# Kernel tuning notes

Measured on AMD Instinct MI355X. Metric: run time of the kernel, lower is better.

The kernel has to match this reference:

```python
import jax, jax.numpy as jnp
import numpy as np

B, S, D = 2, 2048, 1024
H = 8
HD = D // H  # 128
RANK = 4
CONTROL_SCALE = 1.0


def setup_inputs() -> dict:
    key = jax.random.key(0)
    ks = jax.random.split(key, 8)
    sd = 0.02
    return {
        "hidden_states": jax.random.normal(ks[0], (B, S, D), jnp.float32),
        "control_states": jax.random.normal(ks[1], (B, S, D), jnp.float32),
        "Wq": jax.random.normal(ks[2], (D, D), jnp.float32) * sd,
        "Wk": jax.random.normal(ks[3], (D, D), jnp.float32) * sd,
        "Wv": jax.random.normal(ks[4], (D, D), jnp.float32) * sd,
        "Wo": jax.random.normal(ks[5], (D, D), jnp.float32) * sd,
        "bo": jnp.zeros((D,), jnp.float32),
        "lora_down": jax.random.normal(ks[6], (RANK, D), jnp.float32) * sd,
        "lora_up": jax.random.normal(ks[7], (D, RANK), jnp.float32) * sd,
    }


def _split_heads(x):  # [B,S,D] -> [B,H,S,HD]
    return x.reshape(B, S, H, HD).transpose(0, 2, 1, 3)


def reference(hidden_states, control_states, Wq, Wk, Wv, Wo, bo, lora_down, lora_up):
    # q/k/v projections (Linear, no bias); self-attention (encoder_hidden_states=None)
    q = _split_heads(jnp.einsum("bsd,ed->bse", hidden_states, Wq))
    k = _split_heads(jnp.einsum("bsd,ed->bse", hidden_states, Wk))
    v = _split_heads(jnp.einsum("bsd,ed->bse", hidden_states, Wv))
    inv_sqrt_d = 1.0 / jnp.sqrt(jnp.asarray(HD, q.dtype))
    scores = jnp.einsum("bhqd,bhkd->bhqk", q, k) * inv_sqrt_d  # [B,H,S,S]
    probs = jax.nn.softmax(scores, axis=-1)
    attn_out = jnp.einsum("bhqk,bhkd->bhqd", probs, v)  # [B,H,S,HD]
    attn_out = attn_out.transpose(0, 2, 1, 3).reshape(B, S, D)
    # to_out[0] Linear with bias; to_out[1] Dropout is identity at eval
    out = jnp.einsum("bsd,ed->bse", attn_out, Wo) + bo
    # LoRA control injection: up(down(control_states))
    ctrl = jnp.einsum("bsr,er->bse", jnp.einsum("bsd,rd->bsr", control_states, lora_down), lora_up)
    return out + CONTROL_SCALE * ctrl
```

## Files before the change

### kernel.cpp

```cpp
#include <hip/hip_runtime.h>
#include <hip/hip_bf16.h>


typedef __bf16 bf8_t __attribute__((ext_vector_type(8)));
typedef float f32x4 __attribute__((ext_vector_type(4)));

#define MFMA_BF16(a, b, c) __builtin_amdgcn_mfma_f32_16x16x32_bf16((a), (b), (c), 0, 0, 0)

__device__ __forceinline__ void gload_lds16(const void* g, void* l) {
  __builtin_amdgcn_global_load_lds(
      (const __attribute__((address_space(1))) void*)g,
      (__attribute__((address_space(3))) void*)l, 16, 0, 0);
}

__global__ __launch_bounds__(256) void cvt5_k(
    const float* __restrict__ s0, const float* __restrict__ s1,
    const float* __restrict__ s2, const float* __restrict__ s3,
    const float* __restrict__ s4, __bf16* __restrict__ d0,
    __bf16* __restrict__ d1, __bf16* __restrict__ d2, __bf16* __restrict__ d3,
    __bf16* __restrict__ d4) {
  const int which = blockIdx.y;
  const float* s = (which == 0) ? s0 : (which == 1) ? s1 : (which == 2) ? s2
                   : (which == 3) ? s3 : s4;
  __bf16* d = (which == 0) ? d0 : (which == 1) ? d1 : (which == 2) ? d2
              : (which == 3) ? d3 : d4;
  const int n = (which == 0) ? (4096 * 1024) : (1024 * 1024);
  const int i = (blockIdx.x * 256 + threadIdx.x) * 8;
  if (i >= n) return;
  float4 a = *(const float4*)(s + i);
  float4 b = *(const float4*)(s + i + 4);
  bf8_t r;
  r[0] = (__bf16)a.x; r[1] = (__bf16)a.y; r[2] = (__bf16)a.z; r[3] = (__bf16)a.w;
  r[4] = (__bf16)b.x; r[5] = (__bf16)b.y; r[6] = (__bf16)b.z; r[7] = (__bf16)b.w;
  *(bf8_t*)(d + i) = r;
}

__device__ __forceinline__ void gemm_tile(const __bf16* __restrict__ Abase,
                                          const __bf16* __restrict__ Wbase,
                                          int K, __bf16* sA, __bf16* sB,
                                          f32x4 acc[4][4]) {
  const int tid = threadIdx.x;
  const int wave = tid >> 6, lane = tid & 63;
  const int wr = (wave >> 1) * 64, wc = (wave & 1) * 64;
  const int lrow = lane >> 3, lchunk = lane & 7;

  for (int m = 0; m < 4; ++m)
    for (int n = 0; n < 4; ++n)
      acc[m][n] = f32x4{0.f, 0.f, 0.f, 0.f};

  for (int k0 = 0; k0 < K; k0 += 64) {
    for (int i = 0; i < 4; ++i) {
      const int rbase = i * 32 + wave * 8;
      gload_lds16(Abase + (size_t)(rbase + lrow) * K + k0 + lchunk * 8,
                  sA + rbase * 64);
      gload_lds16(Wbase + (size_t)(rbase + lrow) * K + k0 + lchunk * 8,
                  sB + rbase * 64);
    }
    __syncthreads();

    for (int kk = 0; kk < 2; ++kk) {
      bf8_t af[4], bfr[4];
      const int koff = kk * 32 + (lane >> 4) * 8;
      for (int m = 0; m < 4; ++m)
        af[m] = *(const bf8_t*)&sA[(wr + m * 16 + (lane & 15)) * 64 + koff];
      for (int n = 0; n < 4; ++n)
        bfr[n] = *(const bf8_t*)&sB[(wc + n * 16 + (lane & 15)) * 64 + koff];
      for (int m = 0; m < 4; ++m)
        for (int n = 0; n < 4; ++n)
          acc[m][n] = MFMA_BF16(af[m], bfr[n], acc[m][n]);
    }
    __syncthreads();
  }
}

__global__ __launch_bounds__(256) void gemm_qkv_k(
    const __bf16* __restrict__ X, const __bf16* __restrict__ Wq,
    const __bf16* __restrict__ Wk, const __bf16* __restrict__ Wv,
    __bf16* __restrict__ Qb, __bf16* __restrict__ Kb, __bf16* __restrict__ Vtb) {
  __shared__ __bf16 sA[128 * 64];
  __shared__ __bf16 sB[128 * 64];
  const int z = blockIdx.z;
  const int K = 1024;
  int rowT, colT, Nout;
  const __bf16 *Abase, *Wbase;
  __bf16* C;
  if (z == 2) {
    rowT = blockIdx.x; colT = blockIdx.y; Nout = 4096;
    Abase = Wv + (size_t)rowT * 128 * K;
    Wbase = X + (size_t)colT * 128 * K;
    C = Vtb;
  } else {
    rowT = blockIdx.y; colT = blockIdx.x; Nout = 1024;
    Abase = X + (size_t)rowT * 128 * K;
    Wbase = ((z == 0) ? Wq : Wk) + (size_t)colT * 128 * K;
    C = (z == 0) ? Qb : Kb;
  }
  f32x4 acc[4][4];
  gemm_tile(Abase, Wbase, K, sA, sB, acc);

  const int lane = threadIdx.x & 63, wave = threadIdx.x >> 6;
  const int wr = (wave >> 1) * 64, wc = (wave & 1) * 64;
  const int row0 = rowT * 128 + wr + (lane >> 4) * 4;
  const int col0 = colT * 128 + wc + (lane & 15);
  for (int m = 0; m < 4; ++m)
    for (int n = 0; n < 4; ++n)
      for (int j = 0; j < 4; ++j)
        C[(size_t)(row0 + m * 16 + j) * Nout + col0 + n * 16] = (__bf16)acc[m][n][j];
}

__global__ __launch_bounds__(256) void lora_down_k(
    const float* __restrict__ ctrl, const float* __restrict__ down,
    float* __restrict__ tmp) {
  const int tid = threadIdx.x, wave = tid >> 6, lane = tid & 63;
  const int s = blockIdx.x * 4 + wave;
  const float* cp = ctrl + (size_t)s * 1024 + lane * 16;
  float4 c[4];
  for (int i = 0; i < 4; ++i) c[i] = *(const float4*)(cp + i * 4);
  for (int r = 0; r < 4; ++r) {
    const float* dp = down + r * 1024 + lane * 16;
    float acc = 0.f;
    for (int i = 0; i < 4; ++i) {
      float4 dv = *(const float4*)(dp + i * 4);
      acc += c[i].x * dv.x + c[i].y * dv.y + c[i].z * dv.z + c[i].w * dv.w;
    }
    for (int off = 32; off > 0; off >>= 1) acc += __shfl_xor(acc, off);
    if (lane == 0) tmp[s * 4 + r] = acc;
  }
}

__global__ __launch_bounds__(256) void flash_attn_k(
    const __bf16* __restrict__ Qg, const __bf16* __restrict__ Kg,
    const __bf16* __restrict__ Vtg, __bf16* __restrict__ Og) {
  const int S = 2048, D = 1024;
  __shared__ __bf16 sK[2][64 * 128];
  __shared__ __bf16 sVt[2][128 * 64];
  __shared__ __bf16 sP[4][16 * 72];
  const int qt = blockIdx.x, bh = blockIdx.y;
  const int b = bh >> 3, h = bh & 7;
  const int tid = threadIdx.x, wave = tid >> 6, lane = tid & 63;
  const size_t base = (size_t)b * S * D + (size_t)h * 128;
  const size_t vtbase = (size_t)h * 128 * 4096 + (size_t)b * 2048;
  const int q0 = qt * 64 + wave * 16;
  const int g = lane >> 4;
  const int koff = g * 8;

  bf8_t qf[4];
  {
    const float scale = 0.08838834764831845f;
    const __bf16* qp = Qg + base + (size_t)(q0 + (lane & 15)) * D + koff;
    for (int d0 = 0; d0 < 4; ++d0) {
      bf8_t v = *(const bf8_t*)(qp + d0 * 32);
      for (int j = 0; j < 8; ++j) v[j] = (__bf16)((float)v[j] * scale);
      qf[d0] = v;
    }
  }

  f32x4 o[8];
  for (int f = 0; f < 8; ++f) o[f] = f32x4{0.f, 0.f, 0.f, 0.f};
  float mrow[4] = {-1e30f, -1e30f, -1e30f, -1e30f};
  float lrow[4] = {0.f, 0.f, 0.f, 0.f};

  auto stageK = [&](int buf, int kv) {
    for (int i = 0; i < 4; ++i) {
      const int r = i * 16 + wave * 4 + (lane >> 4);
      const int gc = (lane & 15) ^ (r & 7);
      gload_lds16(Kg + base + (size_t)(kv + r) * D + gc * 8,
                  &sK[buf][i * 2048 + wave * 512]);
    }
  };
  auto stageV = [&](int buf, int kv) {
    for (int i = 0; i < 4; ++i) {
      const int r = wave * 32 + i * 8 + (lane >> 3);
      const int gc = (lane & 7) ^ (r & 7);
      gload_lds16(Vtg + vtbase + (size_t)r * 4096 + kv + gc * 8,
                  &sVt[buf][(wave * 32 + i * 8) * 64]);
    }
  };

  stageK(0, 0);
  stageV(0, 0);

  for (int t = 0; t < 32; ++t) {
    const int cur = t & 1;
    __syncthreads();
    if (t < 31) {
      stageK(cur ^ 1, (t + 1) * 64);
      stageV(cur ^ 1, (t + 1) * 64);
    }

    f32x4 s4[4];
    const __bf16* kb_ = sK[cur];
    for (int n = 0; n < 4; ++n) {
      f32x4 a_ = f32x4{0.f, 0.f, 0.f, 0.f};
      const int r = n * 16 + (lane & 15);
      for (int d0 = 0; d0 < 4; ++d0) {
        const int c = (4 * d0 + g) ^ (r & 7);
        a_ = MFMA_BF16(qf[d0], *(const bf8_t*)&kb_[r * 128 + c * 8], a_);
      }
      s4[n] = a_;
    }

    float tmax[4];
    for (int j = 0; j < 4; ++j)
      tmax[j] = fmaxf(fmaxf(s4[0][j], s4[1][j]), fmaxf(s4[2][j], s4[3][j]));
    for (int off = 1; off < 16; off <<= 1)
      for (int j = 0; j < 4; ++j)
        tmax[j] = fmaxf(tmax[j], __shfl_xor(tmax[j], off));
    float sc_[4], rs[4];
    for (int j = 0; j < 4; ++j) {
      float mnew = fmaxf(mrow[j], tmax[j]);
      sc_[j] = __expf(mrow[j] - mnew);
      mrow[j] = mnew;
      rs[j] = 0.f;
    }
    for (int n = 0; n < 4; ++n)
      for (int j = 0; j < 4; ++j) {
        float p = __expf(s4[n][j] - mrow[j]);
        s4[n][j] = p;
        rs[j] += p;
      }
    for (int off = 1; off < 16; off <<= 1)
      for (int j = 0; j < 4; ++j) rs[j] += __shfl_xor(rs[j], off);
    for (int j = 0; j < 4; ++j) lrow[j] = lrow[j] * sc_[j] + rs[j];
    for (int f = 0; f < 8; ++f)
      for (int j = 0; j < 4; ++j) o[f][j] *= sc_[j];

    __bf16* pw = &sP[wave][0];
    for (int n = 0; n < 4; ++n)
      for (int j = 0; j < 4; ++j)
        pw[(g * 4 + j) * 72 + n * 16 + (lane & 15)] = (__bf16)s4[n][j];

    const __bf16* vt_ = sVt[cur];
    for (int kk = 0; kk < 2; ++kk) {
      bf8_t pa = *(const bf8_t*)&pw[(lane & 15) * 72 + kk * 32 + koff];
      for (int f = 0; f < 8; ++f) {
        const int d = f * 16 + (lane & 15);
        const int c = (4 * kk + g) ^ (d & 7);
        bf8_t vb = *(const bf8_t*)&vt_[d * 64 + c * 8];
        o[f] = MFMA_BF16(pa, vb, o[f]);
      }
    }
  }

  float inv[4];
  for (int j = 0; j < 4; ++j) inv[j] = 1.f / lrow[j];
  for (int f = 0; f < 8; ++f)
    for (int j = 0; j < 4; ++j)
      Og[base + (size_t)(q0 + g * 4 + j) * D + f * 16 + (lane & 15)] =
          (__bf16)(o[f][j] * inv[j]);
}

__global__ __launch_bounds__(256) void gemm_out_k(
    const __bf16* __restrict__ A, const __bf16* __restrict__ Wo,
    const float* __restrict__ bo, const float* __restrict__ lup,
    const float* __restrict__ tmp, float* __restrict__ out) {
  __shared__ __bf16 sA[128 * 64];
  __shared__ __bf16 sB[128 * 64];
  const int bcol = blockIdx.x, brow = blockIdx.y;
  const int K = 1024, N = 1024;
  f32x4 acc[4][4];
  gemm_tile(A + (size_t)brow * 128 * K, Wo + (size_t)bcol * 128 * K, K, sA, sB, acc);

  const int lane = threadIdx.x & 63, wave = threadIdx.x >> 6;
  const int wr = (wave >> 1) * 64, wc = (wave & 1) * 64;
  for (int n = 0; n < 4; ++n) {
    const int col = bcol * 128 + wc + n * 16 + (lane & 15);
    const float bias = bo[col];
    const float u0 = lup[col * 4 + 0], u1 = lup[col * 4 + 1];
    const float u2 = lup[col * 4 + 2], u3 = lup[col * 4 + 3];
    for (int m = 0; m < 4; ++m)
      for (int j = 0; j < 4; ++j) {
        const int row = brow * 128 + wr + m * 16 + (lane >> 4) * 4 + j;
        const float* t = tmp + row * 4;
        float v = acc[m][n][j] + bias + t[0] * u0 + t[1] * u1 + t[2] * u2 + t[3] * u3;
        out[(size_t)row * N + col] = v;
      }
  }
}

extern "C" void kernel_launch(void* const* d_in, const int* in_sizes, int n_in,
                              void* d_out, int out_size, void* d_ws, size_t ws_size,
                              hipStream_t stream) {
  (void)in_sizes; (void)n_in; (void)out_size; (void)ws_size;
  const float* hs  = (const float*)d_in[0];
  const float* cs  = (const float*)d_in[1];
  const float* Wq  = (const float*)d_in[2];
  const float* Wk  = (const float*)d_in[3];
  const float* Wv  = (const float*)d_in[4];
  const float* Wo  = (const float*)d_in[5];
  const float* bo  = (const float*)d_in[6];
  const float* ldw = (const float*)d_in[7];
  const float* lup = (const float*)d_in[8];
  float* out = (float*)d_out;

  const size_t MD = (size_t)4096 * 1024;
  const size_t WD = (size_t)1024 * 1024;
  __bf16* hsb = (__bf16*)d_ws;
  __bf16* Wqb = hsb + MD;
  __bf16* Wkb = Wqb + WD;
  __bf16* Wvb = Wkb + WD;
  __bf16* Wob = Wvb + WD;
  __bf16* Qb  = Wob + WD;
  __bf16* Kb  = Qb + MD;
  __bf16* Vtb = Kb + MD;
  __bf16* Ab  = Vtb + MD;
  float*  tmp = (float*)(Ab + MD);

  cvt5_k<<<dim3(2048, 5), 256, 0, stream>>>(hs, Wq, Wk, Wv, Wo,
                                            hsb, Wqb, Wkb, Wvb, Wob);
  gemm_qkv_k<<<dim3(8, 32, 3), 256, 0, stream>>>(hsb, Wqb, Wkb, Wvb, Qb, Kb, Vtb);
  lora_down_k<<<dim3(1024), 256, 0, stream>>>(cs, ldw, tmp);
  flash_attn_k<<<dim3(32, 16), 256, 0, stream>>>(Qb, Kb, Vtb, Ab);
  gemm_out_k<<<dim3(8, 32), 256, 0, stream>>>(Ab, Wob, bo, lup, tmp, out);
}
```

Baseline: 190.6 us.

## Rewrite flash attention with 32x32 MFMA, register-resident P and lazy rescale

The attention kernel now runs two waves per block, each owning 32 query rows, and uses 32x32x16 bf16 MFMA with S computed transposed so each lane holds a single query column. P is packed to bf16 and exchanged between lanes with cross-half shuffles instead of a shared-memory round trip. Softmax uses exp2 with log2e folded into the Q scale, and the output rescale is skipped unless the running max grows by more than 8. The aim is to cut LDS traffic, per-row shuffle reductions and rescale work in the attention kernel. The costs are half as many threads per block, higher register pressure and a tolerance-based lazy rescale.

Result: faster. 176.0 us (-7.7%).

```diff
diff --git a/kernel.cpp b/kernel.cpp
--- a/kernel.cpp
+++ b/kernel.cpp
@@ -4,13 +4,22 @@
 
 typedef __bf16 bf8_t __attribute__((ext_vector_type(8)));
 typedef float f32x4 __attribute__((ext_vector_type(4)));
-
-#define MFMA_BF16(a, b, c) __builtin_amdgcn_mfma_f32_16x16x32_bf16((a), (b), (c), 0, 0, 0)
+typedef float f32x16 __attribute__((ext_vector_type(16)));
+typedef unsigned u32x4 __attribute__((ext_vector_type(4)));
+
+#define MFMA16(a, b, c) __builtin_amdgcn_mfma_f32_16x16x32_bf16((a), (b), (c), 0, 0, 0)
+#define MFMA32(a, b, c) __builtin_amdgcn_mfma_f32_32x32x16_bf16((a), (b), (c), 0, 0, 0)
 
 __device__ __forceinline__ void gload_lds16(const void* g, void* l) {
   __builtin_amdgcn_global_load_lds(
       (const __attribute__((address_space(1))) void*)g,
       (__attribute__((address_space(3))) void*)l, 16, 0, 0);
+}
+
+__device__ __forceinline__ unsigned pk2(float a, float b) {
+  unsigned short ua = __builtin_bit_cast(unsigned short, (__bf16)a);
+  unsigned short ub = __builtin_bit_cast(unsigned short, (__bf16)b);
+  return (unsigned)ua | ((unsigned)ub << 16);
 }
 
 __global__ __launch_bounds__(256) void cvt5_k(
@@ -67,7 +76,7 @@
         bfr[n] = *(const bf8_t*)&sB[(wc + n * 16 + (lane & 15)) * 64 + koff];
       for (int m = 0; m < 4; ++m)
         for (int n = 0; n < 4; ++n)
-          acc[m][n] = MFMA_BF16(af[m], bfr[n], acc[m][n]);
+          acc[m][n] = MFMA16(af[m], bfr[n], acc[m][n]);
     }
     __syncthreads();
   }
@@ -128,52 +137,57 @@
   }
 }
 
-__global__ __launch_bounds__(256) void flash_attn_k(
+__global__ __launch_bounds__(128) void flash_attn_k(
     const __bf16* __restrict__ Qg, const __bf16* __restrict__ Kg,
     const __bf16* __restrict__ Vtg, __bf16* __restrict__ Og) {
   const int S = 2048, D = 1024;
   __shared__ __bf16 sK[2][64 * 128];
   __shared__ __bf16 sVt[2][128 * 64];
-  __shared__ __bf16 sP[4][16 * 72];
+  __shared__ float sW[2][32];
   const int qt = blockIdx.x, bh = blockIdx.y;
   const int b = bh >> 3, h = bh & 7;
   const int tid = threadIdx.x, wave = tid >> 6, lane = tid & 63;
+  const int l31 = lane & 31, hi = lane >> 5;
   const size_t base = (size_t)b * S * D + (size_t)h * 128;
   const size_t vtbase = (size_t)h * 128 * 4096 + (size_t)b * 2048;
-  const int q0 = qt * 64 + wave * 16;
-  const int g = lane >> 4;
-  const int koff = g * 8;
-
-  bf8_t qf[4];
+  const int q0 = qt * 64 + wave * 32;
+
+  bf8_t qf[8];
   {
-    const float scale = 0.08838834764831845f;
-    const __bf16* qp = Qg + base + (size_t)(q0 + (lane & 15)) * D + koff;
-    for (int d0 = 0; d0 < 4; ++d0) {
-      bf8_t v = *(const bf8_t*)(qp + d0 * 32);
-      for (int j = 0; j < 8; ++j) v[j] = (__bf16)((float)v[j] * scale);
-      qf[d0] = v;
-    }
-  }
-
-  f32x4 o[8];
-  for (int f = 0; f < 8; ++f) o[f] = f32x4{0.f, 0.f, 0.f, 0.f};
-  float mrow[4] = {-1e30f, -1e30f, -1e30f, -1e30f};
-  float lrow[4] = {0.f, 0.f, 0.f, 0.f};
+    const float c = 0.08838834764831845f * 1.4426950408889634f;
+    const __bf16* qp = Qg + base + (size_t)(q0 + l31) * D + hi * 8;
+#pragma unroll
+    for (int dc = 0; dc < 8; ++dc) {
+      bf8_t v = *(const bf8_t*)(qp + dc * 16);
+#pragma unroll
+      for (int j = 0; j < 8; ++j) v[j] = (__bf16)((float)v[j] * c);
+      qf[dc] = v;
+    }
+  }
+
+  f32x16 accO[4];
+#pragma unroll
+  for (int db = 0; db < 4; ++db)
+#pragma unroll
+    for (int j = 0; j < 16; ++j) accO[db][j] = 0.f;
+  float m_ = -1e30f, l_ = 0.f;
 
   auto stageK = [&](int buf, int kv) {
-    for (int i = 0; i < 4; ++i) {
-      const int r = i * 16 + wave * 4 + (lane >> 4);
+#pragma unroll
+    for (int i = 0; i < 8; ++i) {
+      const int r = wave * 32 + i * 4 + (lane >> 4);
       const int gc = (lane & 15) ^ (r & 7);
       gload_lds16(Kg + base + (size_t)(kv + r) * D + gc * 8,
-                  &sK[buf][i * 2048 + wave * 512]);
+                  &sK[buf][(wave * 32 + i * 4) * 128]);
     }
   };
   auto stageV = [&](int buf, int kv) {
-    for (int i = 0; i < 4; ++i) {
-      const int r = wave * 32 + i * 8 + (lane >> 3);
-      const int gc = (lane & 7) ^ (r & 7);
-      gload_lds16(Vtg + vtbase + (size_t)r * 4096 + kv + gc * 8,
-                  &sVt[buf][(wave * 32 + i * 8) * 64]);
+#pragma unroll
+    for (int i = 0; i < 8; ++i) {
+      const int d = wave * 64 + i * 8 + (lane >> 3);
+      const int gc = (lane & 7) ^ (d & 7);
+      gload_lds16(Vtg + vtbase + (size_t)d * 4096 + kv + gc * 8,
+                  &sVt[buf][(wave * 64 + i * 8) * 64]);
     }
   };
 
@@ -188,66 +202,99 @@
       stageV(cur ^ 1, (t + 1) * 64);
     }
 
-    f32x4 s4[4];
+    f32x16 accS[2];
+#pragma unroll
+    for (int kb = 0; kb < 2; ++kb)
+#pragma unroll
+      for (int j = 0; j < 16; ++j) accS[kb][j] = 0.f;
     const __bf16* kb_ = sK[cur];
-    for (int n = 0; n < 4; ++n) {
-      f32x4 a_ = f32x4{0.f, 0.f, 0.f, 0.f};
-      const int r = n * 16 + (lane & 15);
-      for (int d0 = 0; d0 < 4; ++d0) {
-        const int c = (4 * d0 + g) ^ (r & 7);
-        a_ = MFMA_BF16(qf[d0], *(const bf8_t*)&kb_[r * 128 + c * 8], a_);
-      }
-      s4[n] = a_;
-    }
-
-    float tmax[4];
-    for (int j = 0; j < 4; ++j)
-      tmax[j] = fmaxf(fmaxf(s4[0][j], s4[1][j]), fmaxf(s4[2][j], s4[3][j]));
-    for (int off = 1; off < 16; off <<= 1)
-      for (int j = 0; j < 4; ++j)
-        tmax[j] = fmaxf(tmax[j], __shfl_xor(tmax[j], off));
-    float sc_[4], rs[4];
-    for (int j = 0; j < 4; ++j) {
-      float mnew = fmaxf(mrow[j], tmax[j]);
-      sc_[j] = __expf(mrow[j] - mnew);
-      mrow[j] = mnew;
-      rs[j] = 0.f;
-    }
-    for (int n = 0; n < 4; ++n)
-      for (int j = 0; j < 4; ++j) {
-        float p = __expf(s4[n][j] - mrow[j]);
-        s4[n][j] = p;
-        rs[j] += p;
-      }
-    for (int off = 1; off < 16; off <<= 1)
-      for (int j = 0; j < 4; ++j) rs[j] += __shfl_xor(rs[j], off);
-    for (int j = 0; j < 4; ++j) lrow[j] = lrow[j] * sc_[j] + rs[j];
-    for (int f = 0; f < 8; ++f)
-      for (int j = 0; j < 4; ++j) o[f][j] *= sc_[j];
-
-    __bf16* pw = &sP[wave][0];
-    for (int n = 0; n < 4; ++n)
-      for (int j = 0; j < 4; ++j)
-        pw[(g * 4 + j) * 72 + n * 16 + (lane & 15)] = (__bf16)s4[n][j];
+#pragma unroll
+    for (int kb = 0; kb < 2; ++kb) {
+      const int kr = kb * 32 + l31;
+#pragma unroll
+      for (int dc = 0; dc < 8; ++dc) {
+        bf8_t a = *(const bf8_t*)&kb_[kr * 128 + ((2 * dc + hi) ^ (kr & 7)) * 8];
+        accS[kb] = MFMA32(a, qf[dc], accS[kb]);
+      }
+    }
+
+    float pm = accS[0][0];
+#pragma unroll
+    for (int j = 1; j < 16; ++j) pm = fmaxf(pm, accS[0][j]);
+#pragma unroll
+    for (int j = 0; j < 16; ++j) pm = fmaxf(pm, accS[1][j]);
+    pm = fmaxf(pm, __shfl_xor(pm, 32));
+
+    if (__ballot(pm > m_ + 8.0f)) {
+      const float mn = fmaxf(m_, pm);
+      const float sc = exp2f(m_ - mn);
+      m_ = mn;
+      l_ *= sc;
+      if (hi == 0) sW[wave][l31] = sc;
+#pragma unroll
+      for (int r = 0; r < 16; ++r) {
+        const float scr = sW[wave][(r & 3) + 8 * (r >> 2) + 4 * hi];
+#pragma unroll
+        for (int db = 0; db < 4; ++db) accO[db][r] *= scr;
+      }
+    }
+
+    float rs = 0.f;
+#pragma unroll
+    for (int kb = 0; kb < 2; ++kb)
+#pragma unroll
+      for (int j = 0; j < 16; ++j) {
+        const float p = exp2f(accS[kb][j] - m_);
+        accS[kb][j] = p;
+        rs += p;
+      }
+    rs += __shfl_xor(rs, 32);
+    l_ += rs;
+
+    unsigned pk[2][4][2];
+#pragma unroll
+    for (int kb = 0; kb < 2; ++kb)
+#pragma unroll
+      for (int tq = 0; tq < 4; ++tq) {
+        pk[kb][tq][0] = pk2(accS[kb][4 * tq + 0], accS[kb][4 * tq + 1]);
+        pk[kb][tq][1] = pk2(accS[kb][4 * tq + 2], accS[kb][4 * tq + 3]);
+      }
 
     const __bf16* vt_ = sVt[cur];
-    for (int kk = 0; kk < 2; ++kk) {
-      bf8_t pa = *(const bf8_t*)&pw[(lane & 15) * 72 + kk * 32 + koff];
-      for (int f = 0; f < 8; ++f) {
-        const int d = f * 16 + (lane & 15);
-        const int c = (4 * kk + g) ^ (d & 7);
-        bf8_t vb = *(const bf8_t*)&vt_[d * 64 + c * 8];
-        o[f] = MFMA_BF16(pa, vb, o[f]);
-      }
-    }
-  }
-
-  float inv[4];
-  for (int j = 0; j < 4; ++j) inv[j] = 1.f / lrow[j];
-  for (int f = 0; f < 8; ++f)
-    for (int j = 0; j < 4; ++j)
-      Og[base + (size_t)(q0 + g * 4 + j) * D + f * 16 + (lane & 15)] =
-          (__bf16)(o[f][j] * inv[j]);
+#pragma unroll
+    for (int kc = 0; kc < 4; ++kc) {
+      const int kb = kc >> 1, par = kc & 1;
+      const unsigned own0 = hi ? pk[kb][2 * par + 1][0] : pk[kb][2 * par][0];
+      const unsigned own1 = hi ? pk[kb][2 * par + 1][1] : pk[kb][2 * par][1];
+      const unsigned snd0 = hi ? pk[kb][2 * par][0] : pk[kb][2 * par + 1][0];
+      const unsigned snd1 = hi ? pk[kb][2 * par][1] : pk[kb][2 * par + 1][1];
+      const unsigned rc0 = (unsigned)__shfl_xor((int)snd0, 32);
+      const unsigned rc1 = (unsigned)__shfl_xor((int)snd1, 32);
+      u32x4 fr;
+      fr[0] = hi ? rc0 : own0;
+      fr[1] = hi ? rc1 : own1;
+      fr[2] = hi ? own0 : rc0;
+      fr[3] = hi ? own1 : rc1;
+      const bf8_t pa = __builtin_bit_cast(bf8_t, fr);
+#pragma unroll
+      for (int db = 0; db < 4; ++db) {
+        const int dr = db * 32 + l31;
+        bf8_t vb = *(const bf8_t*)&vt_[dr * 64 + ((2 * kc + hi) ^ (dr & 7)) * 8];
+        accO[db] = MFMA32(pa, vb, accO[db]);
+      }
+    }
+  }
+
+  if (hi == 0) sW[wave][l31] = l_;
+#pragma unroll
+  for (int r = 0; r < 16; ++r) {
+    const int qr = (r & 3) + 8 * (r >> 2) + 4 * hi;
+    const float linv = 1.0f / sW[wave][qr];
+    __bf16* op = Og + base + (size_t)(q0 + qr) * D + l31;
+#pragma unroll
+    for (int db = 0; db < 4; ++db)
+      op[db * 32] = (__bf16)(accO[db][r] * linv);
+  }
 }
 
 __global__ __launch_bounds__(256) void gemm_out_k(
@@ -310,6 +357,6 @@
                                             hsb, Wqb, Wkb, Wvb, Wob);
   gemm_qkv_k<<<dim3(8, 32, 3), 256, 0, stream>>>(hsb, Wqb, Wkb, Wvb, Qb, Kb, Vtb);
   lora_down_k<<<dim3(1024), 256, 0, stream>>>(cs, ldw, tmp);
-  flash_attn_k<<<dim3(32, 16), 256, 0, stream>>>(Qb, Kb, Vtb, Ab);
+  flash_attn_k<<<dim3(32, 16), 128, 0, stream>>>(Qb, Kb, Vtb, Ab);
   gemm_out_k<<<dim3(8, 32), 256, 0, stream>>>(Ab, Wob, bo, lup, tmp, out);
 }
```
